# Kernel tuning notes

Hardware: AMD Instinct MI355X
Metric: run time of the kernel (lower is better)

## Reference

```python
import jax, jax.numpy as jnp
import numpy as np

N = 50000      # nodes
E = 500000     # edges
F = 128        # node feature dim
ED = 6         # edge feature dim
HID = 64       # hidden per head
HEADS = 4
G = 256        # graphs in batch
NEG_SLOPE = 0.2


def setup_inputs() -> dict:
    key = jax.random.key(0)
    ks = jax.random.split(key, 24)
    s = 0.05
    HC = HEADS * HID
    inp = {
        "x": jax.random.normal(ks[0], (N, F), jnp.float32),
        "edge_index": jax.random.randint(ks[1], (2, E), 0, N, dtype=jnp.int32),
        "edge_attr": jax.random.normal(ks[2], (E, ED), jnp.float32),
        "batch": jnp.sort(jax.random.randint(ks[3], (N,), 0, G, dtype=jnp.int32)),
        # layer 1: in=F, heads=HEADS, concat
        "w_src1": jax.random.normal(ks[4], (F, HC), jnp.float32) * s,
        "w_dst1": jax.random.normal(ks[5], (F, HC), jnp.float32) * s,
        "w_edge1": jax.random.normal(ks[6], (ED, HC), jnp.float32) * s,
        "att1": jax.random.normal(ks[7], (HEADS, HID), jnp.float32) * s,
        "b1": jnp.zeros((HC,), jnp.float32),
        # layer 2: in=HC, heads=HEADS, concat
        "w_src2": jax.random.normal(ks[8], (HC, HC), jnp.float32) * s,
        "w_dst2": jax.random.normal(ks[9], (HC, HC), jnp.float32) * s,
        "w_edge2": jax.random.normal(ks[10], (ED, HC), jnp.float32) * s,
        "att2": jax.random.normal(ks[11], (HEADS, HID), jnp.float32) * s,
        "b2": jnp.zeros((HC,), jnp.float32),
        # layer 3: in=HC, heads=1, concat=False (mean over heads)
        "w_src3": jax.random.normal(ks[12], (HC, HID), jnp.float32) * s,
        "w_dst3": jax.random.normal(ks[13], (HC, HID), jnp.float32) * s,
        "w_edge3": jax.random.normal(ks[14], (ED, HID), jnp.float32) * s,
        "att3": jax.random.normal(ks[15], (1, HID), jnp.float32) * s,
        "b3": jnp.zeros((HID,), jnp.float32),
        # MLP head
        "fc1_w": jax.random.normal(ks[16], (HID, HID), jnp.float32) * s,
        "fc1_b": jnp.zeros((HID,), jnp.float32),
        "out_w": jax.random.normal(ks[17], (HID, 1), jnp.float32) * s,
        "out_b": jnp.zeros((1,), jnp.float32),
    }
    return inp


def _segment_softmax(logits, seg, num_segments):
    # logits: [E, H], per-destination-node softmax
    m = jax.ops.segment_max(logits, seg, num_segments=num_segments)
    m = jnp.where(jnp.isfinite(m), m, 0.0)
    e = jnp.exp(logits - m[seg])
    denom = jax.ops.segment_sum(e, seg, num_segments=num_segments)
    return e / (denom[seg] + 1e-16)


def _gatv2(x, src, dst, edge_attr, w_src, w_dst, w_edge, att, bias, concat):
    H, C = att.shape
    n = x.shape[0]
    xs = (x @ w_src).reshape(n, H, C)            # source transform
    xd = (x @ w_dst).reshape(n, H, C)            # destination transform
    ea = (edge_attr @ w_edge).reshape(-1, H, C)  # edge transform
    xs_e = xs[src]                               # [E,H,C] gather
    z = jax.nn.leaky_relu(xs_e + xd[dst] + ea, NEG_SLOPE)
    logits = jnp.einsum('ehc,hc->eh', z, att)
    alpha = _segment_softmax(logits, dst, n)     # [E,H]
    msg = xs_e * alpha[:, :, None]
    out = jax.ops.segment_sum(msg, dst, num_segments=n)  # [N,H,C]
    out = out.reshape(n, H * C) if concat else out.mean(axis=1)
    return out + bias


def reference(x, edge_index, edge_attr, batch,
              w_src1, w_dst1, w_edge1, att1, b1,
              w_src2, w_dst2, w_edge2, att2, b2,
              w_src3, w_dst3, w_edge3, att3, b3,
              fc1_w, fc1_b, out_w, out_b):
    src, dst = edge_index[0], edge_index[1]
    h = _gatv2(x, src, dst, edge_attr, w_src1, w_dst1, w_edge1, att1, b1, True)
    h = jax.nn.elu(h)
    h = _gatv2(h, src, dst, edge_attr, w_src2, w_dst2, w_edge2, att2, b2, True)
    h = jax.nn.elu(h)
    h = _gatv2(h, src, dst, edge_attr, w_src3, w_dst3, w_edge3, att3, b3, False)
    h = jax.nn.elu(h)
    g = jax.ops.segment_sum(h, batch, num_segments=G)  # global_add_pool
    g = jax.nn.elu(g @ fc1_w + fc1_b)
    return g @ out_w + out_b  # [G, 1]
```

## Files before the change

kernel.cpp:

```cpp
#include <hip/hip_runtime.h>
#include <hip/hip_bf16.h>
#include <cstddef>
#include <cstdint>

constexpr int NN    = 50000;
constexpr int EE    = 500000;
constexpr int FF    = 128;
constexpr int HIDC  = 64;
constexpr int NHEAD = 4;
constexpr int HC    = 256;
constexpr int GG    = 256;

typedef __attribute__((ext_vector_type(2))) float f32x2;
typedef __attribute__((ext_vector_type(4))) float f32x4;
typedef __attribute__((ext_vector_type(8))) short bf16x8;

struct __align__(16) EPack { int soff; int pad; float e0, e1, e2, e3, e4, e5; };

__device__ inline short f2bf(float f) {
  union { float f; unsigned u; } v; v.f = f;
  unsigned r = v.u + 0x7fffu + ((v.u >> 16) & 1u);
  return (short)(r >> 16);
}

__device__ inline void bf4_unpack(uint2 v, f32x2& a, f32x2& b) {
  union { unsigned u; float f; } t;
  t.u = v.x << 16;          a.x = t.f;
  t.u = v.x & 0xffff0000u;  a.y = t.f;
  t.u = v.y << 16;          b.x = t.f;
  t.u = v.y & 0xffff0000u;  b.y = t.f;
}

struct WtJobs {
  const float* w[6];
  short* o[6];
  int K[6], N[6];
  int cum[7];
};

__global__ void prep_all(const float* __restrict__ x, short* __restrict__ xbf,
                         int* __restrict__ deg, float* __restrict__ gp,
                         int* __restrict__ pairs_tail, WtJobs j) {
  int i = blockIdx.x * blockDim.x + threadIdx.x;
  if (i < NN * FF) xbf[i] = f2bf(x[i]);
  if (i < NN) deg[i] = 0;
  if (i < GG * HIDC) gp[i] = 0.f;
  if (i < 16 * 8) pairs_tail[i] = 0;
  if (i < j.cum[6]) {
    int s = 0;
    while (i >= j.cum[s + 1]) s++;
    int li = i - j.cum[s];
    int K = j.K[s], N = j.N[s];
    int n = li / K, k = li - n * K;
    j.o[s][li] = f2bf(j.w[s][k * N + n]);
  }
}

__global__ void count_deg(const int* __restrict__ dst, int* __restrict__ deg) {
  int i = blockIdx.x * blockDim.x + threadIdx.x;
  if (i < EE) atomicAdd(&deg[dst[i]], 1);
}

constexpr int SCAN_T = 256;
constexpr int SCAN_B = 64;
constexpr int SCHUNK = 4;

__global__ __launch_bounds__(SCAN_T) void scan_stage1(const int* __restrict__ deg,
                                                      int* __restrict__ bsum) {
  __shared__ int red[SCAN_T];
  const int t = threadIdx.x, b = blockIdx.x;
  int base = (b * SCAN_T + t) * SCHUNK;
  int s = 0;
  #pragma unroll
  for (int i = 0; i < SCHUNK; i++) {
    int idx = base + i;
    if (idx < NN) s += deg[idx];
  }
  red[t] = s;
  __syncthreads();
  for (int off = SCAN_T / 2; off > 0; off >>= 1) {
    if (t < off) red[t] += red[t + off];
    __syncthreads();
  }
  if (t == 0) bsum[b] = red[0];
}

__global__ __launch_bounds__(64) void scan_stage2(int* __restrict__ bsum) {
  int t = threadIdx.x;
  int v = bsum[t];
  #pragma unroll
  for (int off = 1; off < 64; off <<= 1) {
    int o = __shfl_up(v, off, 64);
    if (t >= off) v += o;
  }
  bsum[t] = v;
}

__global__ __launch_bounds__(SCAN_T) void scan_stage3(const int* __restrict__ deg,
                                                      const int* __restrict__ bsum,
                                                      int* __restrict__ offs,
                                                      int* __restrict__ cur) {
  __shared__ int red[SCAN_T];
  const int t = threadIdx.x, b = blockIdx.x;
  const int base = (b * SCAN_T + t) * SCHUNK;
  int local[SCHUNK];
  int s = 0;
  #pragma unroll
  for (int i = 0; i < SCHUNK; i++) {
    int idx = base + i;
    local[i] = (idx < NN) ? deg[idx] : 0;
    s += local[i];
  }
  red[t] = s;
  __syncthreads();
  for (int off = 1; off < SCAN_T; off <<= 1) {
    int v = (t >= off) ? red[t - off] : 0;
    __syncthreads();
    red[t] += v;
    __syncthreads();
  }
  const int blockBase = (b == 0) ? 0 : bsum[b - 1];
  int run = blockBase + red[t] - s;
  #pragma unroll
  for (int i = 0; i < SCHUNK; i++) {
    int idx = base + i;
    if (idx < NN) {
      offs[idx] = run; cur[idx] = run; run += local[i];
    }
  }
  if (b == SCAN_B - 1 && t == SCAN_T - 1) offs[NN] = run;
}

__global__ void fill_edges(const int* __restrict__ src, const int* __restrict__ dst,
                           const float* __restrict__ eattr,
                           int* __restrict__ cur, EPack* __restrict__ pairs) {
  int i = blockIdx.x * blockDim.x + threadIdx.x;
  if (i < EE) {
    int pos = atomicAdd(&cur[dst[i]], 1);
    const float* ea = eattr + i * 6;
    int4* q = (int4*)(pairs + pos);
    int4 w0, w1;
    w0.x = src[i] * 1024; w0.y = 0;
    w0.z = __float_as_int(ea[0]); w0.w = __float_as_int(ea[1]);
    w1.x = __float_as_int(ea[2]); w1.y = __float_as_int(ea[3]);
    w1.z = __float_as_int(ea[4]); w1.w = __float_as_int(ea[5]);
    q[0] = w0; q[1] = w1;
  }
}

#define APAD 72

__global__ __launch_bounds__(256) void gemm_bf16_v2(
    const short* __restrict__ A,
    const short* __restrict__ Bt,
    short* __restrict__ Cbf,
    int M, int N, int K, int GX, int swz) {
  __shared__ short As[128][APAD];
  int bx, by;
  if (swz) {
    const int id = blockIdx.x;
    const int r = id & 7, u = id >> 3;
    by = u & 3;
    bx = ((u >> 2) << 3) | r;
    if (bx >= GX) return;
  } else {
    bx = blockIdx.x; by = blockIdx.y;
  }
  const int tid  = threadIdx.x;
  const int wave = tid >> 6;
  const int lane = tid & 63;
  const int quad = lane >> 4;
  const int l16  = lane & 15;
  const int wr   = wave >> 1;
  const int wc   = wave & 1;
  const int bm = bx * 128;
  const int bn = by * 128;

  const int srow = tid >> 3;
  const int skc  = (tid & 7) * 8;

  const short* Bw = Bt + (size_t)(bn + wc * 64 + l16) * K + quad * 8;

  f32x4 acc[4][4];
  #pragma unroll
  for (int i = 0; i < 4; i++)
    #pragma unroll
    for (int jj = 0; jj < 4; jj++) acc[i][jj] = (f32x4){0, 0, 0, 0};

  for (int k0 = 0; k0 < K; k0 += 64) {
    #pragma unroll
    for (int i = 0; i < 4; i++) {
      int r = srow + i * 32;
      int gm = bm + r;
      int4 av = {0, 0, 0, 0};
      if (gm < M) av = *(const int4*)(A + (size_t)gm * K + k0 + skc);
      *(int4*)(&As[r][skc]) = av;
    }
    __syncthreads();

    #pragma unroll
    for (int kq = 0; kq < 2; kq++) {
      bf16x8 bfr[4];
      #pragma unroll
      for (int ni = 0; ni < 4; ni++)
        bfr[ni] = *(const bf16x8*)(Bw + (size_t)(ni * 16) * K + k0 + kq * 32);
      bf16x8 af[4];
      #pragma unroll
      for (int mi = 0; mi < 4; mi++)
        af[mi] = *(const bf16x8*)(&As[wr * 64 + mi * 16 + l16][kq * 32 + quad * 8]);
      #pragma unroll
      for (int mi = 0; mi < 4; mi++)
        #pragma unroll
        for (int ni = 0; ni < 4; ni++)
          acc[mi][ni] = __builtin_amdgcn_mfma_f32_16x16x32_bf16(af[mi], bfr[ni], acc[mi][ni], 0, 0, 0);
    }
    __syncthreads();
  }

  #pragma unroll
  for (int mi = 0; mi < 4; mi++) {
    #pragma unroll
    for (int r = 0; r < 4; r++) {
      int gm = bm + wr * 64 + mi * 16 + quad * 4 + r;
      if (gm < M) {
        #pragma unroll
        for (int ni = 0; ni < 4; ni++)
          Cbf[(size_t)gm * N + bn + wc * 64 + ni * 16 + l16] = f2bf(acc[mi][ni][r]);
      }
    }
  }
}

template <int CHS, int SOFF_SHR>
__global__ __launch_bounds__(256) void gat_fused_v6(
    const short* __restrict__ xs, const short* __restrict__ xd,
    const EPack* __restrict__ pairs, const float* __restrict__ w_edge,
    const float* __restrict__ att, const float* __restrict__ bias,
    const int* __restrict__ offs, short* __restrict__ out_bf) {
  const int tid  = threadIdx.x;
  const int wv   = tid >> 6;
  const int lane = tid & 63;
  const int ch   = lane * 4;

  const f32x4 attf = *(const f32x4*)(att + ch);
  f32x4 wef[6];
  #pragma unroll
  for (int k = 0; k < 6; k++) wef[k] = *(const f32x4*)(w_edge + k * 256 + ch);
  const f32x4 b4 = *(const f32x4*)(bias + ch);

  const char* xs_b = (const char*)xs + ch * 2;

  const int n = blockIdx.x * 4 + wv;

  uint2 xdr = *(const uint2*)(xd + (size_t)n * CHS + ch);
  f32x2 xd01, xd23; bf4_unpack(xdr, xd01, xd23);

  const int beg = offs[n], end = offs[n + 1];
  float l = 0.f;
  f32x2 acc01 = {0, 0}, acc23 = {0, 0};

  int idx = beg;
  if (idx < end) {
    const int4* pp = (const int4*)(pairs + idx);
    int4 a0 = pp[0], b0 = pp[1];
    const int4* pq = (const int4*)(pairs + idx + 1);
    int4 a1 = pq[0], b1 = pq[1];
    uint2 g0 = *(const uint2*)(xs_b + ((unsigned)a0.x >> SOFF_SHR));
    while (idx < end) {
      idx += 1;
      uint2 g1 = *(const uint2*)(xs_b + ((unsigned)a1.x >> SOFF_SHR));
      const int4* pn = (const int4*)(pairs + idx + 1);
      int4 a2 = pn[0], b2 = pn[1];

      f32x2 x01, x23; bf4_unpack(g0, x01, x23);
      f32x2 e01 = {__int_as_float(a0.z), __int_as_float(a0.w)};
      f32x2 e23 = {__int_as_float(b0.x), __int_as_float(b0.y)};
      f32x2 e45 = {__int_as_float(b0.z), __int_as_float(b0.w)};
      f32x2 z01 = x01 + xd01, z23 = x23 + xd23;
      z01 = __builtin_elementwise_fma((f32x2)(e01.x), wef[0].xy, z01);
      z23 = __builtin_elementwise_fma((f32x2)(e01.x), wef[0].zw, z23);
      z01 = __builtin_elementwise_fma((f32x2)(e01.y), wef[1].xy, z01);
      z23 = __builtin_elementwise_fma((f32x2)(e01.y), wef[1].zw, z23);
      z01 = __builtin_elementwise_fma((f32x2)(e23.x), wef[2].xy, z01);
      z23 = __builtin_elementwise_fma((f32x2)(e23.x), wef[2].zw, z23);
      z01 = __builtin_elementwise_fma((f32x2)(e23.y), wef[3].xy, z01);
      z23 = __builtin_elementwise_fma((f32x2)(e23.y), wef[3].zw, z23);
      z01 = __builtin_elementwise_fma((f32x2)(e45.x), wef[4].xy, z01);
      z23 = __builtin_elementwise_fma((f32x2)(e45.x), wef[4].zw, z23);
      z01 = __builtin_elementwise_fma((f32x2)(e45.y), wef[5].xy, z01);
      z23 = __builtin_elementwise_fma((f32x2)(e45.y), wef[5].zw, z23);
      z01 = __builtin_elementwise_max(z01, z01 * 0.2f);
      z23 = __builtin_elementwise_max(z23, z23 * 0.2f);
      f32x2 d = z01 * attf.xy;
      d = __builtin_elementwise_fma(z23, attf.zw, d);
      float p = d.x + d.y;
      #pragma unroll
      for (int off = 1; off < 16; off <<= 1) p += __shfl_xor(p, off, 64);

      float wgt = __expf(p);
      l += wgt;
      acc01 = __builtin_elementwise_fma((f32x2)wgt, x01, acc01);
      acc23 = __builtin_elementwise_fma((f32x2)wgt, x23, acc23);

      a0 = a1; b0 = b1; a1 = a2; b1 = b2; g0 = g1;
    }
  }

  float inv = 1.f / (l + 1e-16f);
  float v0 = acc01.x * inv + b4.x;
  float v1 = acc01.y * inv + b4.y;
  float v2 = acc23.x * inv + b4.z;
  float v3 = acc23.y * inv + b4.w;
  v0 = v0 > 0.f ? v0 : (__expf(v0) - 1.f);
  v1 = v1 > 0.f ? v1 : (__expf(v1) - 1.f);
  v2 = v2 > 0.f ? v2 : (__expf(v2) - 1.f);
  v3 = v3 > 0.f ? v3 : (__expf(v3) - 1.f);
  short4 o;
  o.x = f2bf(v0); o.y = f2bf(v1); o.z = f2bf(v2); o.w = f2bf(v3);
  *(short4*)(out_bf + (size_t)n * 256 + ch) = o;
}

__global__ __launch_bounds__(256) void gat_fused_pool4(
    const short* __restrict__ xs, const short* __restrict__ xd,
    const EPack* __restrict__ pairs, const float* __restrict__ w_edge,
    const float* __restrict__ att, const float* __restrict__ bias,
    const int* __restrict__ offs, const int* __restrict__ batch,
    float* __restrict__ gp) {
  constexpr int CHS = 128;
  const int lane = threadIdx.x & 63;
  const int slot = lane >> 4;
  const int pos  = lane & 15;
  const int ch   = pos * 4;
  const int nbase = blockIdx.x * 16 + (threadIdx.x >> 6) * 4;

  const f32x4 attf = *(const f32x4*)(att + ch);
  f32x4 wef[6];
  #pragma unroll
  for (int k = 0; k < 6; k++) wef[k] = *(const f32x4*)(w_edge + k * 64 + ch);
  const f32x4 b4 = *(const f32x4*)(bias + ch);

  const char* xs_b = (const char*)xs + ch * 2;

  #pragma unroll
  for (int nn = 0; nn < 4; nn++) {
    const int n = nbase + nn;
    if (n >= NN) break;

    uint2 xdr = *(const uint2*)(xd + (size_t)n * CHS + ch);
    f32x2 xd01, xd23; bf4_unpack(xdr, xd01, xd23);

    const int beg = offs[n], end = offs[n + 1];
    float l = 0.f;
    f32x2 acc01 = {0, 0}, acc23 = {0, 0};

    if (beg < end) {
      const int niter = (end - beg + 3) >> 2;
      int idx = beg + slot;
      bool v = idx < end;
      const int4* pp = (const int4*)(pairs + idx);
      int4 a = pp[0], b = pp[1];
      uint2 xr = *(const uint2*)(xs_b + ((unsigned)a.x >> 2));

      for (int it = 0; it < niter; it++) {
        int4 ac = a, bc = b;
        uint2 xrc = xr;
        bool vc = v;
        idx += 4;
        v = idx < end;
        pp = (const int4*)(pairs + idx);
        a = pp[0]; b = pp[1];
        xr = *(const uint2*)(xs_b + ((unsigned)a.x >> 2));

        f32x2 x01, x23; bf4_unpack(xrc, x01, x23);
        f32x2 e01 = {__int_as_float(ac.z), __int_as_float(ac.w)};
        f32x2 e23 = {__int_as_float(bc.x), __int_as_float(bc.y)};
        f32x2 e45 = {__int_as_float(bc.z), __int_as_float(bc.w)};
        f32x2 z01 = x01 + xd01, z23 = x23 + xd23;
        z01 = __builtin_elementwise_fma((f32x2)(e01.x), wef[0].xy, z01);
        z23 = __builtin_elementwise_fma((f32x2)(e01.x), wef[0].zw, z23);
        z01 = __builtin_elementwise_fma((f32x2)(e01.y), wef[1].xy, z01);
        z23 = __builtin_elementwise_fma((f32x2)(e01.y), wef[1].zw, z23);
        z01 = __builtin_elementwise_fma((f32x2)(e23.x), wef[2].xy, z01);
        z23 = __builtin_elementwise_fma((f32x2)(e23.x), wef[2].zw, z23);
        z01 = __builtin_elementwise_fma((f32x2)(e23.y), wef[3].xy, z01);
        z23 = __builtin_elementwise_fma((f32x2)(e23.y), wef[3].zw, z23);
        z01 = __builtin_elementwise_fma((f32x2)(e45.x), wef[4].xy, z01);
        z23 = __builtin_elementwise_fma((f32x2)(e45.x), wef[4].zw, z23);
        z01 = __builtin_elementwise_fma((f32x2)(e45.y), wef[5].xy, z01);
        z23 = __builtin_elementwise_fma((f32x2)(e45.y), wef[5].zw, z23);
        z01 = __builtin_elementwise_max(z01, z01 * 0.2f);
        z23 = __builtin_elementwise_max(z23, z23 * 0.2f);
        f32x2 d = z01 * attf.xy;
        d = __builtin_elementwise_fma(z23, attf.zw, d);
        float p = d.x + d.y;
        #pragma unroll
        for (int off = 1; off < 16; off <<= 1) p += __shfl_xor(p, off, 64);

        float w = vc ? __expf(p) : 0.f;
        l += w;
        acc01 = __builtin_elementwise_fma((f32x2)w, x01, acc01);
        acc23 = __builtin_elementwise_fma((f32x2)w, x23, acc23);
      }
    }

    #pragma unroll
    for (int d = 16; d <= 32; d <<= 1) {
      l       += __shfl_xor(l, d, 64);
      acc01.x += __shfl_xor(acc01.x, d, 64);
      acc01.y += __shfl_xor(acc01.y, d, 64);
      acc23.x += __shfl_xor(acc23.x, d, 64);
      acc23.y += __shfl_xor(acc23.y, d, 64);
    }

    if (slot == 0) {
      float inv = 1.f / (l + 1e-16f);
      float v0 = acc01.x * inv + b4.x;
      float v1 = acc01.y * inv + b4.y;
      float v2 = acc23.x * inv + b4.z;
      float v3 = acc23.y * inv + b4.w;
      v0 = v0 > 0.f ? v0 : (__expf(v0) - 1.f);
      v1 = v1 > 0.f ? v1 : (__expf(v1) - 1.f);
      v2 = v2 > 0.f ? v2 : (__expf(v2) - 1.f);
      v3 = v3 > 0.f ? v3 : (__expf(v3) - 1.f);
      float* g = gp + (size_t)batch[n] * 64 + ch;
      atomicAdd(g + 0, v0);
      atomicAdd(g + 1, v1);
      atomicAdd(g + 2, v2);
      atomicAdd(g + 3, v3);
    }
  }
}

__global__ __launch_bounds__(64) void head_mlp(const float* __restrict__ gpool,
                                               const float* __restrict__ fc1_w,
                                               const float* __restrict__ fc1_b,
                                               const float* __restrict__ out_w,
                                               const float* __restrict__ out_b,
                                               float* __restrict__ out) {
  int gr = blockIdx.x;
  int c = threadIdx.x;
  float acc = fc1_b[c];
  #pragma unroll 8
  for (int k = 0; k < HIDC; k++)
    acc += gpool[gr * HIDC + k] * fc1_w[k * HIDC + c];
  acc = acc > 0.f ? acc : (__expf(acc) - 1.f);
  float v = acc * out_w[c];
  #pragma unroll
  for (int off = 32; off > 0; off >>= 1) v += __shfl_xor(v, off, 64);
  if (c == 0) out[gr] = v + out_b[0];
}

extern "C" void kernel_launch(void* const* d_in, const int* in_sizes, int n_in,
                              void* d_out, int out_size, void* d_ws, size_t ws_size,
                              hipStream_t stream) {
  const float* x      = (const float*)d_in[0];
  const int*   ei     = (const int*)d_in[1];
  const float* eattr  = (const float*)d_in[2];
  const int*   batch  = (const int*)d_in[3];
  const float* w_src1 = (const float*)d_in[4];
  const float* w_dst1 = (const float*)d_in[5];
  const float* w_edge1= (const float*)d_in[6];
  const float* att1   = (const float*)d_in[7];
  const float* b1     = (const float*)d_in[8];
  const float* w_src2 = (const float*)d_in[9];
  const float* w_dst2 = (const float*)d_in[10];
  const float* w_edge2= (const float*)d_in[11];
  const float* att2   = (const float*)d_in[12];
  const float* b2     = (const float*)d_in[13];
  const float* w_src3 = (const float*)d_in[14];
  const float* w_dst3 = (const float*)d_in[15];
  const float* w_edge3= (const float*)d_in[16];
  const float* att3   = (const float*)d_in[17];
  const float* b3     = (const float*)d_in[18];
  const float* fc1_w  = (const float*)d_in[19];
  const float* fc1_b  = (const float*)d_in[20];
  const float* out_w  = (const float*)d_in[21];
  const float* out_b  = (const float*)d_in[22];

  const int* src = ei;
  const int* dst = ei + EE;

  char* p = (char*)d_ws;
  auto carve = [&](size_t bytes) -> void* {
    void* r = (void*)p;
    p += (bytes + 255) & ~(size_t)255;
    return r;
  };
  short* xsd_bf = (short*)carve((size_t)NN * 512 * sizeof(short));
  short* xbf1   = (short*)carve((size_t)NN * FF * sizeof(short));
  short* hbf    = (short*)carve((size_t)NN * HC * sizeof(short));
  short* wtcat1 = (short*)carve((size_t)512 * FF * sizeof(short));
  short* wtcat2 = (short*)carve((size_t)512 * HC * sizeof(short));
  short* wtcat3 = (short*)carve((size_t)128 * HC * sizeof(short));
  float* gp     = (float*)carve((size_t)GG * HIDC * sizeof(float));
  int* deg      = (int*)carve((size_t)NN * sizeof(int));
  int* offs     = (int*)carve((size_t)(NN + 1) * sizeof(int));
  int* cur      = (int*)carve((size_t)NN * sizeof(int));
  int* bsum     = (int*)carve((size_t)SCAN_B * sizeof(int));
  EPack* pairs  = (EPack*)carve((size_t)(EE + 16) * sizeof(EPack));
  (void)ws_size; (void)n_in; (void)in_sizes; (void)out_size;

  const int GM128 = (NN + 127) / 128;
  const int GSWZ  = 8 * 4 * ((GM128 + 7) / 8);

  WtJobs j;
  j.w[0] = w_src1; j.o[0] = wtcat1;                       j.K[0] = FF; j.N[0] = HC;
  j.w[1] = w_dst1; j.o[1] = wtcat1 + (size_t)HC * FF;     j.K[1] = FF; j.N[1] = HC;
  j.w[2] = w_src2; j.o[2] = wtcat2;                       j.K[2] = HC; j.N[2] = HC;
  j.w[3] = w_dst2; j.o[3] = wtcat2 + (size_t)HC * HC;     j.K[3] = HC; j.N[3] = HC;
  j.w[4] = w_src3; j.o[4] = wtcat3;                       j.K[4] = HC; j.N[4] = HIDC;
  j.w[5] = w_dst3; j.o[5] = wtcat3 + (size_t)HIDC * HC;   j.K[5] = HC; j.N[5] = HIDC;
  j.cum[0] = 0;
  for (int s = 0; s < 6; s++) j.cum[s + 1] = j.cum[s] + j.K[s] * j.N[s];
  prep_all<<<(NN * FF + 255) / 256, 256, 0, stream>>>(x, xbf1, deg, gp,
                                                      (int*)(pairs + EE), j);

  count_deg<<<(EE + 255) / 256, 256, 0, stream>>>(dst, deg);
  scan_stage1<<<SCAN_B, SCAN_T, 0, stream>>>(deg, bsum);
  scan_stage2<<<1, 64, 0, stream>>>(bsum);
  scan_stage3<<<SCAN_B, SCAN_T, 0, stream>>>(deg, bsum, offs, cur);
  fill_edges<<<(EE + 255) / 256, 256, 0, stream>>>(src, dst, eattr, cur, pairs);

  gemm_bf16_v2<<<dim3(GSWZ), 256, 0, stream>>>(xbf1, wtcat1, xsd_bf, NN, 512, FF,
                                               GM128, 1);
  gat_fused_v6<512, 0><<<NN / 4, 256, 0, stream>>>(xsd_bf, xsd_bf + HC, pairs,
                                                   w_edge1, att1, b1, offs, hbf);

  gemm_bf16_v2<<<dim3(GSWZ), 256, 0, stream>>>(hbf, wtcat2, xsd_bf, NN, 512, HC,
                                               GM128, 1);
  gat_fused_v6<512, 0><<<NN / 4, 256, 0, stream>>>(xsd_bf, xsd_bf + HC, pairs,
                                                   w_edge2, att2, b2, offs, hbf);

  gemm_bf16_v2<<<dim3(GM128, 1), 256, 0, stream>>>(hbf, wtcat3, xsd_bf, NN, 128, HC,
                                                   GM128, 0);
  gat_fused_pool4<<<(NN + 15) / 16, 256, 0, stream>>>(xsd_bf, xsd_bf + HIDC, pairs,
                                                      w_edge3, att3, b3, offs, batch, gp);

  head_mlp<<<GG, 64, 0, stream>>>(gp, fc1_w, fc1_b, out_w, out_b, (float*)d_out);
}
```

Before: 515.1 us.

## Deepen edge prefetch in GAT layers and remap final layer to one node per group

The layer 1/2 attention kernel now keeps edge records two steps ahead and source-feature gathers one step further ahead, so more memory latency is hidden per wave. The final-layer pooled kernel is restructured: instead of each wave looping over 4 nodes with 4 lane groups splitting one node's edges and a cross-group shuffle reduction, each 16-lane group now owns one node and walks its edges serially, with no per-node reduction or masking. This raises node-level parallelism and removes shuffles, at the cost of more atomics issued concurrently and less balance across high-degree nodes. The grid drops the bounds check, which relies on the node count being divisible by 16.

Measured after the change: 568.2 us. 10.3% more time.

```diff
diff --git a/kernel.cpp b/kernel.cpp
--- a/kernel.cpp
+++ b/kernel.cpp
@@ -232,7 +232,7 @@
 }
 
 template <int CHS, int SOFF_SHR>
-__global__ __launch_bounds__(256) void gat_fused_v6(
+__global__ __launch_bounds__(256) void gat_fused_v7(
     const short* __restrict__ xs, const short* __restrict__ xd,
     const EPack* __restrict__ pairs, const float* __restrict__ w_edge,
     const float* __restrict__ att, const float* __restrict__ bias,
@@ -261,16 +261,19 @@
 
   int idx = beg;
   if (idx < end) {
-    const int4* pp = (const int4*)(pairs + idx);
-    int4 a0 = pp[0], b0 = pp[1];
-    const int4* pq = (const int4*)(pairs + idx + 1);
-    int4 a1 = pq[0], b1 = pq[1];
+    const int4* p0 = (const int4*)(pairs + idx);
+    int4 a0 = p0[0], b0 = p0[1];
+    const int4* p1 = (const int4*)(pairs + idx + 1);
+    int4 a1 = p1[0], b1 = p1[1];
+    const int4* p2 = (const int4*)(pairs + idx + 2);
+    int4 a2 = p2[0], b2 = p2[1];
     uint2 g0 = *(const uint2*)(xs_b + ((unsigned)a0.x >> SOFF_SHR));
+    uint2 g1 = *(const uint2*)(xs_b + ((unsigned)a1.x >> SOFF_SHR));
     while (idx < end) {
       idx += 1;
-      uint2 g1 = *(const uint2*)(xs_b + ((unsigned)a1.x >> SOFF_SHR));
-      const int4* pn = (const int4*)(pairs + idx + 1);
-      int4 a2 = pn[0], b2 = pn[1];
+      uint2 g2 = *(const uint2*)(xs_b + ((unsigned)a2.x >> SOFF_SHR));
+      const int4* pn = (const int4*)(pairs + idx + 2);
+      int4 a3 = pn[0], b3 = pn[1];
 
       f32x2 x01, x23; bf4_unpack(g0, x01, x23);
       f32x2 e01 = {__int_as_float(a0.z), __int_as_float(a0.w)};
@@ -302,7 +305,8 @@
       acc01 = __builtin_elementwise_fma((f32x2)wgt, x01, acc01);
       acc23 = __builtin_elementwise_fma((f32x2)wgt, x23, acc23);
 
-      a0 = a1; b0 = b1; a1 = a2; b1 = b2; g0 = g1;
+      a0 = a1; b0 = b1; a1 = a2; b1 = b2; a2 = a3; b2 = b3;
+      g0 = g1; g1 = g2;
     }
   }
 
@@ -320,18 +324,17 @@
   *(short4*)(out_bf + (size_t)n * 256 + ch) = o;
 }
 
-__global__ __launch_bounds__(256) void gat_fused_pool4(
+__global__ __launch_bounds__(256) void gat_pool_v6(
     const short* __restrict__ xs, const short* __restrict__ xd,
     const EPack* __restrict__ pairs, const float* __restrict__ w_edge,
     const float* __restrict__ att, const float* __restrict__ bias,
     const int* __restrict__ offs, const int* __restrict__ batch,
     float* __restrict__ gp) {
-  constexpr int CHS = 128;
   const int lane = threadIdx.x & 63;
-  const int slot = lane >> 4;
+  const int grp  = lane >> 4;
   const int pos  = lane & 15;
   const int ch   = pos * 4;
-  const int nbase = blockIdx.x * 16 + (threadIdx.x >> 6) * 4;
+  const int n = blockIdx.x * 16 + (threadIdx.x >> 6) * 4 + grp;
 
   const f32x4 attf = *(const f32x4*)(att + ch);
   f32x4 wef[6];
@@ -341,94 +344,74 @@
 
   const char* xs_b = (const char*)xs + ch * 2;
 
-  #pragma unroll
-  for (int nn = 0; nn < 4; nn++) {
-    const int n = nbase + nn;
-    if (n >= NN) break;
-
-    uint2 xdr = *(const uint2*)(xd + (size_t)n * CHS + ch);
-    f32x2 xd01, xd23; bf4_unpack(xdr, xd01, xd23);
-
-    const int beg = offs[n], end = offs[n + 1];
-    float l = 0.f;
-    f32x2 acc01 = {0, 0}, acc23 = {0, 0};
-
-    if (beg < end) {
-      const int niter = (end - beg + 3) >> 2;
-      int idx = beg + slot;
-      bool v = idx < end;
-      const int4* pp = (const int4*)(pairs + idx);
-      int4 a = pp[0], b = pp[1];
-      uint2 xr = *(const uint2*)(xs_b + ((unsigned)a.x >> 2));
-
-      for (int it = 0; it < niter; it++) {
-        int4 ac = a, bc = b;
-        uint2 xrc = xr;
-        bool vc = v;
-        idx += 4;
-        v = idx < end;
-        pp = (const int4*)(pairs + idx);
-        a = pp[0]; b = pp[1];
-        xr = *(const uint2*)(xs_b + ((unsigned)a.x >> 2));
-
-        f32x2 x01, x23; bf4_unpack(xrc, x01, x23);
-        f32x2 e01 = {__int_as_float(ac.z), __int_as_float(ac.w)};
-        f32x2 e23 = {__int_as_float(bc.x), __int_as_float(bc.y)};
-        f32x2 e45 = {__int_as_float(bc.z), __int_as_float(bc.w)};
-        f32x2 z01 = x01 + xd01, z23 = x23 + xd23;
-        z01 = __builtin_elementwise_fma((f32x2)(e01.x), wef[0].xy, z01);
-        z23 = __builtin_elementwise_fma((f32x2)(e01.x), wef[0].zw, z23);
-        z01 = __builtin_elementwise_fma((f32x2)(e01.y), wef[1].xy, z01);
-        z23 = __builtin_elementwise_fma((f32x2)(e01.y), wef[1].zw, z23);
-        z01 = __builtin_elementwise_fma((f32x2)(e23.x), wef[2].xy, z01);
-        z23 = __builtin_elementwise_fma((f32x2)(e23.x), wef[2].zw, z23);
-        z01 = __builtin_elementwise_fma((f32x2)(e23.y), wef[3].xy, z01);
-        z23 = __builtin_elementwise_fma((f32x2)(e23.y), wef[3].zw, z23);
-        z01 = __builtin_elementwise_fma((f32x2)(e45.x), wef[4].xy, z01);
-        z23 = __builtin_elementwise_fma((f32x2)(e45.x), wef[4].zw, z23);
-        z01 = __builtin_elementwise_fma((f32x2)(e45.y), wef[5].xy, z01);
-        z23 = __builtin_elementwise_fma((f32x2)(e45.y), wef[5].zw, z23);
-        z01 = __builtin_elementwise_max(z01, z01 * 0.2f);
-        z23 = __builtin_elementwise_max(z23, z23 * 0.2f);
-        f32x2 d = z01 * attf.xy;
-        d = __builtin_elementwise_fma(z23, attf.zw, d);
-        float p = d.x + d.y;
-        #pragma unroll
-        for (int off = 1; off < 16; off <<= 1) p += __shfl_xor(p, off, 64);
-
-        float w = vc ? __expf(p) : 0.f;
-        l += w;
-        acc01 = __builtin_elementwise_fma((f32x2)w, x01, acc01);
-        acc23 = __builtin_elementwise_fma((f32x2)w, x23, acc23);
-      }
+  uint2 xdr = *(const uint2*)(xd + (size_t)n * 128 + ch);
+  f32x2 xd01, xd23; bf4_unpack(xdr, xd01, xd23);
+
+  const int beg = offs[n], end = offs[n + 1];
+  float l = 0.f;
+  f32x2 acc01 = {0, 0}, acc23 = {0, 0};
+
+  int idx = beg;
+  if (idx < end) {
+    const int4* p0 = (const int4*)(pairs + idx);
+    int4 a0 = p0[0], b0 = p0[1];
+    const int4* p1 = (const int4*)(pairs + idx + 1);
+    int4 a1 = p1[0], b1 = p1[1];
+    uint2 g0 = *(const uint2*)(xs_b + ((unsigned)a0.x >> 2));
+    while (idx < end) {
+      idx += 1;
+      uint2 g1 = *(const uint2*)(xs_b + ((unsigned)a1.x >> 2));
+      const int4* pn = (const int4*)(pairs + idx + 1);
+      int4 a2 = pn[0], b2 = pn[1];
+
+      f32x2 x01, x23; bf4_unpack(g0, x01, x23);
+      f32x2 e01 = {__int_as_float(a0.z), __int_as_float(a0.w)};
+      f32x2 e23 = {__int_as_float(b0.x), __int_as_float(b0.y)};
+      f32x2 e45 = {__int_as_float(b0.z), __int_as_float(b0.w)};
+      f32x2 z01 = x01 + xd01, z23 = x23 + xd23;
+      z01 = __builtin_elementwise_fma((f32x2)(e01.x), wef[0].xy, z01);
+      z23 = __builtin_elementwise_fma((f32x2)(e01.x), wef[0].zw, z23);
+      z01 = __builtin_elementwise_fma((f32x2)(e01.y), wef[1].xy, z01);
+      z23 = __builtin_elementwise_fma((f32x2)(e01.y), wef[1].zw, z23);
+      z01 = __builtin_elementwise_fma((f32x2)(e23.x), wef[2].xy, z01);
+      z23 = __builtin_elementwise_fma((f32x2)(e23.x), wef[2].zw, z23);
+      z01 = __builtin_elementwise_fma((f32x2)(e23.y), wef[3].xy, z01);
+      z23 = __builtin_elementwise_fma((f32x2)(e23.y), wef[3].zw, z23);
+      z01 = __builtin_elementwise_fma((f32x2)(e45.x), wef[4].xy, z01);
+      z23 = __builtin_elementwise_fma((f32x2)(e45.x), wef[4].zw, z23);
+      z01 = __builtin_elementwise_fma((f32x2)(e45.y), wef[5].xy, z01);
+      z23 = __builtin_elementwise_fma((f32x2)(e45.y), wef[5].zw, z23);
+      z01 = __builtin_elementwise_max(z01, z01 * 0.2f);
+      z23 = __builtin_elementwise_max(z23, z23 * 0.2f);
+      f32x2 d = z01 * attf.xy;
+      d = __builtin_elementwise_fma(z23, attf.zw, d);
+      float p = d.x + d.y;
+      #pragma unroll
+      for (int off = 1; off < 16; off <<= 1) p += __shfl_xor(p, off, 64);
+
+      float wgt = __expf(p);
+      l += wgt;
+      acc01 = __builtin_elementwise_fma((f32x2)wgt, x01, acc01);
+      acc23 = __builtin_elementwise_fma((f32x2)wgt, x23, acc23);
+
+      a0 = a1; b0 = b1; a1 = a2; b1 = b2; g0 = g1;
     }
-
-    #pragma unroll
-    for (int d = 16; d <= 32; d <<= 1) {
-      l       += __shfl_xor(l, d, 64);
-      acc01.x += __shfl_xor(acc01.x, d, 64);
-      acc01.y += __shfl_xor(acc01.y, d, 64);
-      acc23.x += __shfl_xor(acc23.x, d, 64);
-      acc23.y += __shfl_xor(acc23.y, d, 64);
-    }
-
-    if (slot == 0) {
-      float inv = 1.f / (l + 1e-16f);
-      float v0 = acc01.x * inv + b4.x;
-      float v1 = acc01.y * inv + b4.y;
-      float v2 = acc23.x * inv + b4.z;
-      float v3 = acc23.y * inv + b4.w;
-      v0 = v0 > 0.f ? v0 : (__expf(v0) - 1.f);
-      v1 = v1 > 0.f ? v1 : (__expf(v1) - 1.f);
-      v2 = v2 > 0.f ? v2 : (__expf(v2) - 1.f);
-      v3 = v3 > 0.f ? v3 : (__expf(v3) - 1.f);
-      float* g = gp + (size_t)batch[n] * 64 + ch;
-      atomicAdd(g + 0, v0);
-      atomicAdd(g + 1, v1);
-      atomicAdd(g + 2, v2);
-      atomicAdd(g + 3, v3);
-    }
-  }
+  }
+
+  float inv = 1.f / (l + 1e-16f);
+  float v0 = acc01.x * inv + b4.x;
+  float v1 = acc01.y * inv + b4.y;
+  float v2 = acc23.x * inv + b4.z;
+  float v3 = acc23.y * inv + b4.w;
+  v0 = v0 > 0.f ? v0 : (__expf(v0) - 1.f);
+  v1 = v1 > 0.f ? v1 : (__expf(v1) - 1.f);
+  v2 = v2 > 0.f ? v2 : (__expf(v2) - 1.f);
+  v3 = v3 > 0.f ? v3 : (__expf(v3) - 1.f);
+  float* g = gp + (size_t)batch[n] * 64 + ch;
+  atomicAdd(g + 0, v0);
+  atomicAdd(g + 1, v1);
+  atomicAdd(g + 2, v2);
+  atomicAdd(g + 3, v3);
 }
 
 __global__ __launch_bounds__(64) void head_mlp(const float* __restrict__ gpool,
@@ -523,18 +506,18 @@
 
   gemm_bf16_v2<<<dim3(GSWZ), 256, 0, stream>>>(xbf1, wtcat1, xsd_bf, NN, 512, FF,
                                                GM128, 1);
-  gat_fused_v6<512, 0><<<NN / 4, 256, 0, stream>>>(xsd_bf, xsd_bf + HC, pairs,
+  gat_fused_v7<512, 0><<<NN / 4, 256, 0, stream>>>(xsd_bf, xsd_bf + HC, pairs,
                                                    w_edge1, att1, b1, offs, hbf);
 
   gemm_bf16_v2<<<dim3(GSWZ), 256, 0, stream>>>(hbf, wtcat2, xsd_bf, NN, 512, HC,
                                                GM128, 1);
-  gat_fused_v6<512, 0><<<NN / 4, 256, 0, stream>>>(xsd_bf, xsd_bf + HC, pairs,
+  gat_fused_v7<512, 0><<<NN / 4, 256, 0, stream>>>(xsd_bf, xsd_bf + HC, pairs,
                                                    w_edge2, att2, b2, offs, hbf);
 
   gemm_bf16_v2<<<dim3(GM128, 1), 256, 0, stream>>>(hbf, wtcat3, xsd_bf, NN, 128, HC,
                                                    GM128, 0);
-  gat_fused_pool4<<<(NN + 15) / 16, 256, 0, stream>>>(xsd_bf, xsd_bf + HIDC, pairs,
-                                                      w_edge3, att3, b3, offs, batch, gp);
+  gat_pool_v6<<<NN / 16, 256, 0, stream>>>(xsd_bf, xsd_bf + HIDC, pairs,
+                                           w_edge3, att3, b3, offs, batch, gp);
 
   head_mlp<<<GG, 64, 0, stream>>>(gp, fc1_w, fc1_b, out_w, out_b, (float*)d_out);
 }
```
